# Kernel tuning notes

Hardware: AMD Instinct MI355X
Metric: run time of the kernel (lower is better)

Reference implementation:

```python
import jax, jax.numpy as jnp
import numpy as np

N = 4096
DIN, DOUT, HID, CUTS = 16, 16, 16, 8
RADIUS = 9.0
SCALES = (1.0, 2.0, 3.0, 5.0, 10.0)
REG = 0.01
CHUNK = 512
GROUPS = 4
DINF = DIN + 2 * len(SCALES)  # 26


def leaky(v):
    return jnp.where(v >= 0, v, 0.2 * v)


def sqdist(a, b):
    d2 = jnp.sum(a * a, -1)[:, None] + jnp.sum(b * b, -1)[None, :] - 2.0 * (a @ b.T)
    return jnp.maximum(d2, 0.0)


def tangent_vectors(n):
    # Duff et al. branchless orthonormal basis, as in dMaSIF geometry_processing
    x, y, z = n[..., 0], n[..., 1], n[..., 2]
    s = jnp.where(z >= 0, 1.0, -1.0)
    a = -1.0 / (s + z)
    b = x * y * a
    t1 = jnp.stack([1.0 + s * x * x * a, s * b, -s * x], -1)
    t2 = jnp.stack([b, s + y * y * a, -y], -1)
    return jnp.stack([t1, t2], axis=-2)  # (..., 2, 3)


def group_norm(x, w, b, eps=1e-5):
    # torch GroupNorm(4, C) applied on (1, C, N): normalize over (C/G, N) per group
    n, c = x.shape
    xt = x.T.reshape(GROUPS, c // GROUPS, n)
    m = jnp.mean(xt, axis=(1, 2), keepdims=True)
    v = jnp.mean((xt - m) ** 2, axis=(1, 2), keepdims=True)
    xt = (xt - m) / jnp.sqrt(v + eps)
    return (xt.reshape(c, n) * w[:, None] + b[:, None]).T


def curvature_features(verts, normals):
    # dMaSIF curvatures(): per-scale Gaussian-window covariances, shape operator S = PPt^-1 PQt
    # Pairwise sums factorized into matmuls with the (N,N) window (no (N,N,8) intermediates).
    n_pts = verts.shape[0]
    d2 = sqdist(verts, verts)
    xx = (verts[:, :, None] * verts[:, None, :]).reshape(n_pts, 9)
    feats = []
    for s in SCALES:
        w = jnp.exp(-d2 / (2.0 * s * s))
        u_n = w @ normals  # scale-smoothed normals
        ns = u_n / jnp.maximum(jnp.linalg.norm(u_n, axis=-1, keepdims=True), 1e-12)
        uv = tangent_vectors(ns)  # (N,2,3)
        s0 = jnp.sum(w, 1)
        sx = w @ verts
        sn = w @ ns
        sxx = (w @ xx).reshape(n_pts, 3, 3)
        xn = (verts[:, :, None] * ns[:, None, :]).reshape(n_pts, 9)
        sxn = (w @ xn).reshape(n_pts, 3, 3)
        # sum_j w_ij (x_j-x_i)(x_j-x_i)^T  and  sum_j w_ij (x_j-x_i)(n_j-n_i)^T
        cxx = sxx - verts[:, :, None] * sx[:, None, :] - sx[:, :, None] * verts[:, None, :] \
              + s0[:, None, None] * verts[:, :, None] * verts[:, None, :]
        cxn = sxn - verts[:, :, None] * sn[:, None, :] - sx[:, :, None] * ns[:, None, :] \
              + s0[:, None, None] * verts[:, :, None] * ns[:, None, :]
        ppt = jnp.einsum('nka,nab,nlb->nkl', uv, cxx, uv) + REG * jnp.eye(2, dtype=verts.dtype)
        pqt = jnp.einsum('nka,nab,nlb->nkl', uv, cxn, uv)
        S = jnp.linalg.solve(ppt, pqt)  # (N,2,2)
        feats.append(jnp.clip(S[:, 0, 0] + S[:, 1, 1], -1.0, 1.0))            # mean curvature
        feats.append(jnp.clip(S[:, 0, 0] * S[:, 1, 1] - S[:, 0, 1] * S[:, 1, 0], -1.0, 1.0))  # gauss
    return jnp.stack(feats, -1)  # (N, 2*len(SCALES))


def _forward(verts, vnormals, x, os_w1, os_b1, os_w2, os_b2,
             ni_w1, ni_b1, ni_w2, ni_b2, gn_in_w, gn_in_b,
             cv_a1, cv_b1, cv_a2, cv_b2, no_w1, no_b1, no_w2, no_b2,
             gn_out_w, gn_out_b, ll_w1, ll_b1, ll_w2, ll_b2, lt_w, lt_b):
    curv = curvature_features(verts, vnormals)
    xf = jnp.concatenate([x, curv], axis=-1)  # (N, DINF)
    w = leaky(xf @ os_w1.T + os_b1) @ os_w2.T + os_b2  # orientation scores (N,1)

    # --- load_mesh: steer tangent frames along the gradient of w ---
    p = verts / RADIUS
    ndot = vnormals @ vnormals.T
    W = jnp.exp(-sqdist(p, p) * (2.0 - ndot) ** 2)  # pseudo-geodesic Gaussian window
    uv = tangent_vectors(vnormals)  # (N,2,3)
    ov3 = W @ (w * p) - (W @ w) * p  # sum_j W_ij w_j (x_j - x_i), factorized
    ov = jnp.einsum('nkd,nd->nk', uv, ov3) + 1e-5
    u = ov / jnp.sqrt(jnp.sum(ov * ov, -1, keepdims=True))
    ex, ey = u[:, 0:1], u[:, 1:2]
    u0, v0 = uv[:, 0], uv[:, 1]
    nuv = jnp.concatenate([vnormals[:, None, :],
                           (ex * u0 + ey * v0)[:, None, :],
                           (-ey * u0 + ex * v0)[:, None, :]], axis=1)  # (N,3,3)

    # --- dMaSIFConv layer ---
    h = leaky(leaky(xf @ ni_w1.T + ni_b1) @ ni_w2.T + ni_b2)
    h = group_norm(h, gn_in_w, gn_in_b)  # (N, HID)
    n_all = nuv[:, 0]
    nc = N // CHUNK
    pc = p.reshape(nc, CHUNK, 3)
    nuvc = nuv.reshape(nc, CHUNK, 3, 3)

    def block(args):
        pi, nuvi = args  # (C,3), (C,3,3)
        dx = p[None, :, :] - pi[:, None, :]  # (C,N,3)
        d2 = jnp.sum(dx * dx, -1)
        win = jnp.exp(-d2 * (2.0 - nuvi[:, 0] @ n_all.T) ** 2)  # (C,N)
        X = jnp.einsum('ckd,cnd->cnk', nuvi, dx)  # local coords (C,N,3)
        y = jax.nn.relu(X @ cv_a1.T + cv_b1) @ cv_a2.T + cv_b2  # filter MLP (C,N,HID)
        return jnp.einsum('cn,cnh,nh->ch', win, y, h)

    xi = jax.lax.map(jax.checkpoint(block), (pc, nuvc)).reshape(N, HID)
    xi = group_norm(leaky(leaky(xi @ no_w1.T + no_b1) @ no_w2.T + no_b2), gn_out_w, gn_out_b)
    xi = jax.nn.relu(xi @ ll_w1.T + ll_b1) @ ll_w2.T + ll_b2  # linear_layers[0]
    return xf @ lt_w.T + lt_b + xi  # linear_transform skip + conv branch


def setup_inputs():
    key = jax.random.key(0)
    ks = jax.random.split(key, 20)

    def lin(k, o, i):
        wk = jax.random.fold_in(k, 0)
        bk = jax.random.fold_in(k, 1)
        return ((1.0 / np.sqrt(i)) * jax.random.normal(wk, (o, i)),
                0.01 * jax.random.normal(bk, (o,)))

    verts = 10.0 * jax.random.normal(ks[0], (N, 3))
    vn = jax.random.normal(ks[1], (N, 3))
    vnormals = vn / jnp.linalg.norm(vn, axis=-1, keepdims=True)
    x = jax.random.normal(ks[2], (N, DIN))
    os_w1, os_b1 = lin(ks[3], DOUT, DINF)
    os_w2, os_b2 = lin(ks[4], 1, DOUT)
    ni_w1, ni_b1 = lin(ks[5], HID, DINF)
    ni_w2, ni_b2 = lin(ks[6], HID, HID)
    cv_a1 = jax.random.normal(ks[7], (CUTS, 3))
    cv_b1 = jax.random.uniform(ks[8], (CUTS,)) * 0.8 * jnp.sqrt(jnp.sum(cv_a1 ** 2, -1))
    cv_a2 = jax.random.uniform(ks[9], (HID, CUTS), minval=-1.0, maxval=1.0) / np.sqrt(CUTS)
    cv_b2 = jax.random.normal(ks[10], (HID,)) * 0.5 * jnp.sqrt(jnp.sum(cv_a2 ** 2, -1))
    no_w1, no_b1 = lin(ks[11], DOUT, HID)
    no_w2, no_b2 = lin(ks[12], DOUT, DOUT)
    ll_w1, ll_b1 = lin(ks[13], DOUT, DOUT)
    ll_w2, ll_b2 = lin(ks[14], DOUT, DOUT)
    lt_w, lt_b = lin(ks[15], DOUT, DINF)
    return {'verts': verts, 'vnormals': vnormals, 'x': x,
            'os_w1': os_w1, 'os_b1': os_b1, 'os_w2': os_w2, 'os_b2': os_b2,
            'ni_w1': ni_w1, 'ni_b1': ni_b1, 'ni_w2': ni_w2, 'ni_b2': ni_b2,
            'gn_in_w': jnp.ones(HID), 'gn_in_b': jnp.zeros(HID),
            'cv_a1': cv_a1, 'cv_b1': cv_b1, 'cv_a2': cv_a2, 'cv_b2': cv_b2,
            'no_w1': no_w1, 'no_b1': no_b1, 'no_w2': no_w2, 'no_b2': no_b2,
            'gn_out_w': jnp.ones(DOUT), 'gn_out_b': jnp.zeros(DOUT),
            'll_w1': ll_w1, 'll_b1': ll_b1, 'll_w2': ll_w2, 'll_b2': ll_b2,
            'lt_w': lt_w, 'lt_b': lt_b}


def reference(verts, vnormals, x, os_w1, os_b1, os_w2, os_b2,
              ni_w1, ni_b1, ni_w2, ni_b2, gn_in_w, gn_in_b,
              cv_a1, cv_b1, cv_a2, cv_b2, no_w1, no_b1, no_w2, no_b2,
              gn_out_w, gn_out_b, ll_w1, ll_b1, ll_w2, ll_b2, lt_w, lt_b):
    return _forward(verts, vnormals, x, os_w1, os_b1, os_w2, os_b2,
                    ni_w1, ni_b1, ni_w2, ni_b2, gn_in_w, gn_in_b,
                    cv_a1, cv_b1, cv_a2, cv_b2, no_w1, no_b1, no_w2, no_b2,
                    gn_out_w, gn_out_b, ll_w1, ll_b1, ll_w2, ll_b2, lt_w, lt_b)
```

## Files before the change

### kernel.cpp

```cpp
#include <hip/hip_runtime.h>
#include <hip/hip_bf16.h>
#include <math.h>

#define NPTS 4096
#define DINF 26
#define LOG2E 1.44269504088896f
#define CSTR 72

typedef float f32x4v __attribute__((ext_vector_type(4)));
typedef __bf16 bf16x8v __attribute__((ext_vector_type(8)));

__device__ __forceinline__ float ldb(const float* p, int i){ return p[i]; }
__device__ __forceinline__ float lk(float v){ return v >= 0.0f ? v : 0.2f*v; }
__device__ __forceinline__ float wsum64(float v){
#pragma unroll
  for(int o=32;o>0;o>>=1) v += __shfl_down(v,o);
  return v;
}
__device__ __forceinline__ unsigned short f2bf(float f){
  return __builtin_bit_cast(unsigned short, __float2bfloat16(f));
}
__device__ __forceinline__ float bf2f(unsigned short u){
  return __bfloat162float(__builtin_bit_cast(__hip_bfloat16, u));
}
__device__ __forceinline__ void wave_lds_fence(){
  __builtin_amdgcn_wave_barrier();
  __builtin_amdgcn_s_waitcnt(0xC07F);
  __builtin_amdgcn_wave_barrier();
}
__device__ __forceinline__ void tangent(float nx,float ny,float nz,float* t1,float* t2){
  float s = (nz >= 0.0f) ? 1.0f : -1.0f;
  float a = -1.0f/(s+nz);
  float b = nx*ny*a;
  t1[0]=1.0f+s*nx*nx*a; t1[1]=s*b; t1[2]=-s*nx;
  t2[0]=b; t2[1]=s+ny*ny*a; t2[2]=-ny;
}

__global__ __launch_bounds__(256) void k0_convert(const float* __restrict__ verts,
                                                  const float* __restrict__ vnorm,
                                                  const float* __restrict__ x,
                                                  float* __restrict__ vertsF,
                                                  float* __restrict__ nF,
                                                  float* __restrict__ pF,
                                                  float* __restrict__ xfF){
  int i = blockIdx.x*blockDim.x + threadIdx.x;
  if(i >= NPTS) return;
#pragma unroll
  for(int d=0;d<3;d++){
    float v = verts[i*3+d];
    vertsF[i*3+d]=v;
    pF[i*3+d]=v*(1.0f/9.0f);
    nF[i*3+d]=vnorm[i*3+d];
  }
#pragma unroll
  for(int c=0;c<16;c++) xfF[i*DINF+c]=x[i*16+c];
}

__global__ __launch_bounds__(512) void k1m(const float* __restrict__ vertsF,
                                           const float* __restrict__ nF,
                                           float* __restrict__ sc){
  __shared__ __align__(16) unsigned short fbh[8][16][CSTR];
  __shared__ __align__(16) unsigned short fbl[8][16][CSTR];
  __shared__ __align__(16) float vq[8][64][4];
  __shared__ float red[8][16][16];
  const float c2e[5] = {0.5f*LOG2E, 0.125f*LOG2E, (1.0f/18.0f)*LOG2E,
                        0.02f*LOG2E, 0.005f*LOG2E};
  int lane = threadIdx.x & 63, w = threadIdx.x >> 6;
  int c16 = lane & 15, q = lane >> 4;
  int it = blockIdx.x >> 1, jh = blockIdx.x & 1;
  int i0 = it*16;
  int ia = i0 + c16;
  float vix=vertsF[ia*3+0], viy=vertsF[ia*3+1], viz=vertsF[ia*3+2];
  float nsqi = vix*vix+viy*viy+viz*viz;
  fbh[w][0][lane]=0x3F80u; fbl[w][0][lane]=0u;
#pragma unroll
  for(int c=13;c<16;c++){ fbh[w][c][lane]=0u; fbl[w][c][lane]=0u; }
  f32x4v acc[5];
#pragma unroll
  for(int s=0;s<5;s++) acc[s] = (f32x4v){0.0f,0.0f,0.0f,0.0f};

  int jbeg = jh*2048 + w*256;
#pragma unroll 1
  for(int jb = jbeg; jb < jbeg+256; jb += 64){
    int j = jb + lane;
    float vx=vertsF[j*3+0], vy=vertsF[j*3+1], vz=vertsF[j*3+2];
    float nx=nF[j*3+0], ny=nF[j*3+1], nz=nF[j*3+2];
    float nsq = vx*vx+vy*vy+vz*vz;
    float fv[13];
    fv[1]=vx; fv[2]=vy; fv[3]=vz;
    fv[4]=vx*vx; fv[5]=vx*vy; fv[6]=vx*vz; fv[7]=vy*vy; fv[8]=vy*vz; fv[9]=vz*vz;
    fv[10]=nx; fv[11]=ny; fv[12]=nz;
#pragma unroll
    for(int c=1;c<13;c++){
      unsigned short h=f2bf(fv[c]);
      fbh[w][c][lane]=h;
      fbl[w][c][lane]=f2bf(fv[c]-bf2f(h));
    }
    *(float4*)&vq[w][lane][0] = make_float4(vx,vy,vz,nsq);
    wave_lds_fence();
#pragma unroll
    for(int q2=0;q2<2;q2++){
      int rb = q2*32 + q*8;
      bf16x8v bh = *(const bf16x8v*)&fbh[w][c16][rb];
      bf16x8v bl = *(const bf16x8v*)&fbl[w][c16][rb];
      bf16x8v af[5];
#pragma unroll
      for(int t=0;t<8;t++){
        float4 vv = *(const float4*)&vq[w][rb+t][0];
        float dot = vix*vv.x + viy*vv.y + viz*vv.z;
        float d2 = fmaxf(nsqi + vv.w - 2.0f*dot, 0.0f);
#pragma unroll
        for(int s=0;s<5;s++)
          af[s][t] = __builtin_bit_cast(__bf16, f2bf(exp2f(-d2*c2e[s])));
      }
#pragma unroll
      for(int s=0;s<5;s++){
        acc[s] = __builtin_amdgcn_mfma_f32_16x16x32_bf16(af[s], bh, acc[s], 0,0,0);
        acc[s] = __builtin_amdgcn_mfma_f32_16x16x32_bf16(af[s], bl, acc[s], 0,0,0);
      }
    }
    wave_lds_fence();
  }
#pragma unroll
  for(int s=0;s<5;s++){
#pragma unroll
    for(int r=0;r<4;r++) red[w][q*4+r][c16] = acc[s][r];
    __syncthreads();
    if(w==0){
      float* base = sc + (size_t)s*13*NPTS;
#pragma unroll
      for(int r=0;r<4;r++){
        int m = q*4+r, i = i0+m;
        float D = 0.0f;
#pragma unroll
        for(int ww=0;ww<8;ww++) D += red[ww][m][c16];
        if(c16==0)       atomicAdd(&base[i], D);
        else if(c16<4)   atomicAdd(&base[NPTS + i*3 + (c16-1)], D);
        else if(c16<10)  atomicAdd(&base[4*NPTS + i*6 + (c16-4)], D);
        else if(c16<13)  atomicAdd(&base[10*NPTS + i*3 + (c16-10)], D);
      }
    }
    __syncthreads();
  }
}

__global__ __launch_bounds__(512) void k2m(const float* __restrict__ vertsF,
                                           const float* __restrict__ sc,
                                           float* __restrict__ mom2){
  __shared__ __align__(16) unsigned short fbh[8][16][CSTR];
  __shared__ __align__(16) unsigned short fbl[8][16][CSTR];
  __shared__ __align__(16) float vq[8][64][4];
  __shared__ float red[8][16][16];
  const float c2e[5] = {0.5f*LOG2E, 0.125f*LOG2E, (1.0f/18.0f)*LOG2E,
                        0.02f*LOG2E, 0.005f*LOG2E};
  int lane = threadIdx.x & 63, w = threadIdx.x >> 6;
  int c16 = lane & 15, q = lane >> 4;
  int it = blockIdx.x >> 1, jh = blockIdx.x & 1;
  int i0 = it*16;
  int ia = i0 + c16;
  float vix=vertsF[ia*3+0], viy=vertsF[ia*3+1], viz=vertsF[ia*3+2];
  float nsqi = vix*vix+viy*viy+viz*viz;
#pragma unroll
  for(int c=12;c<16;c++){ fbh[w][c][lane]=0u; fbl[w][c][lane]=0u; }
  f32x4v acc[5];
#pragma unroll
  for(int s=0;s<5;s++) acc[s] = (f32x4v){0.0f,0.0f,0.0f,0.0f};

  int jbeg = jh*2048 + w*256;
#pragma unroll 1
  for(int jb = jbeg; jb < jbeg+256; jb += 64){
    int j = jb + lane;
    float vx=vertsF[j*3+0], vy=vertsF[j*3+1], vz=vertsF[j*3+2];
    float nsq = vx*vx+vy*vy+vz*vz;
    *(float4*)&vq[w][lane][0] = make_float4(vx,vy,vz,nsq);
    wave_lds_fence();
    float d2c[2][8];
#pragma unroll
    for(int q2=0;q2<2;q2++)
#pragma unroll
      for(int t=0;t<8;t++){
        float4 vv = *(const float4*)&vq[w][q2*32+q*8+t][0];
        float dot = vix*vv.x + viy*vv.y + viz*vv.z;
        d2c[q2][t] = fmaxf(nsqi + vv.w - 2.0f*dot, 0.0f);
      }
    wave_lds_fence();
#pragma unroll
    for(int s=0;s<5;s++){
      const float* ub = sc + (size_t)s*13*NPTS + 10*NPTS + (size_t)j*3;
      float ux=ub[0], uy=ub[1], uz=ub[2];
      float inv = 1.0f/fmaxf(sqrtf(ux*ux+uy*uy+uz*uz), 1e-12f);
      float n0=ux*inv, n1=uy*inv, n2=uz*inv;
      float fv[12];
      fv[0]=n0; fv[1]=n1; fv[2]=n2;
      fv[3]=vx*n0; fv[4]=vx*n1; fv[5]=vx*n2;
      fv[6]=vy*n0; fv[7]=vy*n1; fv[8]=vy*n2;
      fv[9]=vz*n0; fv[10]=vz*n1; fv[11]=vz*n2;
#pragma unroll
      for(int c=0;c<12;c++){
        unsigned short h=f2bf(fv[c]);
        fbh[w][c][lane]=h;
        fbl[w][c][lane]=f2bf(fv[c]-bf2f(h));
      }
      wave_lds_fence();
#pragma unroll
      for(int q2=0;q2<2;q2++){
        int rb = q2*32 + q*8;
        bf16x8v bh = *(const bf16x8v*)&fbh[w][c16][rb];
        bf16x8v bl = *(const bf16x8v*)&fbl[w][c16][rb];
        bf16x8v af;
#pragma unroll
        for(int t=0;t<8;t++)
          af[t] = __builtin_bit_cast(__bf16, f2bf(exp2f(-d2c[q2][t]*c2e[s])));
        acc[s] = __builtin_amdgcn_mfma_f32_16x16x32_bf16(af, bh, acc[s], 0,0,0);
        acc[s] = __builtin_amdgcn_mfma_f32_16x16x32_bf16(af, bl, acc[s], 0,0,0);
      }
      wave_lds_fence();
    }
  }
#pragma unroll
  for(int s=0;s<5;s++){
#pragma unroll
    for(int r=0;r<4;r++) red[w][q*4+r][c16] = acc[s][r];
    __syncthreads();
    if(w==0){
#pragma unroll
      for(int r=0;r<4;r++){
        int m = q*4+r, i = i0+m;
        float D = 0.0f;
#pragma unroll
        for(int ww=0;ww<8;ww++) D += red[ww][m][c16];
        if(c16<12) atomicAdd(&mom2[((size_t)s*NPTS + i)*12 + c16], D);
      }
    }
    __syncthreads();
  }
}

__global__ __launch_bounds__(256) void k2s(const float* __restrict__ vertsF,
                                           const float* __restrict__ sc,
                                           const float* __restrict__ mom2,
                                           float* __restrict__ xfF){
  int idx = blockIdx.x*256 + threadIdx.x;
  int i = idx & (NPTS-1);
  int s = idx >> 12;
  const float* base = sc + (size_t)s*13*NPTS;
  float v[3] = { vertsF[i*3+0], vertsF[i*3+1], vertsF[i*3+2] };
  float s0 = base[i];
  float sx[3] = { base[NPTS+i*3+0], base[NPTS+i*3+1], base[NPTS+i*3+2] };
  float sxx6[6];
#pragma unroll
  for(int k=0;k<6;k++) sxx6[k]=base[4*NPTS+i*6+k];
  float ux=base[10*NPTS+i*3+0], uy=base[10*NPTS+i*3+1], uz=base[10*NPTS+i*3+2];
  float invn = 1.0f/fmaxf(sqrtf(ux*ux+uy*uy+uz*uz), 1e-12f);
  float nsi[3] = { ux*invn, uy*invn, uz*invn };
  const float* M2 = mom2 + ((size_t)s*NPTS + i)*12;
  float sn[3] = { M2[0], M2[1], M2[2] };
  float sxn[3][3];
#pragma unroll
  for(int a=0;a<3;a++)
#pragma unroll
    for(int b=0;b<3;b++) sxn[a][b]=M2[3+a*3+b];
  const int m6[3][3]={{0,1,2},{1,3,4},{2,4,5}};
  float cxx[3][3], cxn[3][3];
#pragma unroll
  for(int a=0;a<3;a++)
#pragma unroll
    for(int b=0;b<3;b++){
      cxx[a][b]=sxx6[m6[a][b]] - v[a]*sx[b] - sx[a]*v[b] + s0*v[a]*v[b];
      cxn[a][b]=sxn[a][b]    - v[a]*sn[b] - sx[a]*nsi[b] + s0*v[a]*nsi[b];
    }
  float t1[3],t2[3];
  tangent(nsi[0],nsi[1],nsi[2],t1,t2);
  float ppt[2][2], pqt[2][2];
#pragma unroll
  for(int k=0;k<2;k++){
    const float* tk = (k==0)?t1:t2;
#pragma unroll
    for(int l=0;l<2;l++){
      const float* tl = (l==0)?t1:t2;
      float accx=0.0f, accn=0.0f;
#pragma unroll
      for(int a=0;a<3;a++)
#pragma unroll
        for(int b=0;b<3;b++){
          accx += tk[a]*cxx[a][b]*tl[b];
          accn += tk[a]*cxn[a][b]*tl[b];
        }
      ppt[k][l]=accx + ((k==l)?0.01f:0.0f);
      pqt[k][l]=accn;
    }
  }
  float det = ppt[0][0]*ppt[1][1]-ppt[0][1]*ppt[1][0];
  float id = 1.0f/det;
  float S00=( ppt[1][1]*pqt[0][0]-ppt[0][1]*pqt[1][0])*id;
  float S01=( ppt[1][1]*pqt[0][1]-ppt[0][1]*pqt[1][1])*id;
  float S10=(-ppt[1][0]*pqt[0][0]+ppt[0][0]*pqt[1][0])*id;
  float S11=(-ppt[1][0]*pqt[0][1]+ppt[0][0]*pqt[1][1])*id;
  float f0=fminf(fmaxf(S00+S11,-1.0f),1.0f);
  float f1=fminf(fmaxf(S00*S11-S01*S10,-1.0f),1.0f);
  xfF[i*DINF+16+2*s]=f0;
  xfF[i*DINF+17+2*s]=f1;
}

__global__ __launch_bounds__(256) void k3_mlps(const float* __restrict__ xfF,
    const float* os_w1, const float* os_b1, const float* os_w2, const float* os_b2,
    const float* ni_w1, const float* ni_b1, const float* ni_w2, const float* ni_b2,
    float* __restrict__ wOS, float* __restrict__ hPre, float* __restrict__ stats){
  int i = blockIdx.x*256 + threadIdx.x;
  int lane = threadIdx.x & 63;
  float xf[DINF];
#pragma unroll
  for(int k=0;k<DINF;k++) xf[k]=xfF[i*DINF+k];
  float h1[16];
#pragma unroll
  for(int o=0;o<16;o++){
    float t=ldb(os_b1,o);
#pragma unroll
    for(int k=0;k<DINF;k++) t += xf[k]*ldb(os_w1,o*DINF+k);
    h1[o]=lk(t);
  }
  float w=ldb(os_b2,0);
#pragma unroll
  for(int o=0;o<16;o++) w += h1[o]*ldb(os_w2,o);
  wOS[i]=w;
#pragma unroll
  for(int o=0;o<16;o++){
    float t=ldb(ni_b1,o);
#pragma unroll
    for(int k=0;k<DINF;k++) t += xf[k]*ldb(ni_w1,o*DINF+k);
    h1[o]=lk(t);
  }
  float h2[16];
#pragma unroll
  for(int o=0;o<16;o++){
    float t=ldb(ni_b2,o);
#pragma unroll
    for(int k=0;k<16;k++) t += h1[k]*ldb(ni_w2,o*16+k);
    h2[o]=lk(t);
    hPre[i*16+o]=h2[o];
  }
  float gs[4]={0,0,0,0}, gq[4]={0,0,0,0};
#pragma unroll
  for(int c=0;c<16;c++){ gs[c>>2]+=h2[c]; gq[c>>2]+=h2[c]*h2[c]; }
  __shared__ float ls[8];
  if(threadIdx.x<8) ls[threadIdx.x]=0.0f;
  __syncthreads();
#pragma unroll
  for(int g=0;g<4;g++){ gs[g]=wsum64(gs[g]); gq[g]=wsum64(gq[g]); }
  if(lane==0){
#pragma unroll
    for(int g=0;g<4;g++){ atomicAdd(&ls[2*g],gs[g]); atomicAdd(&ls[2*g+1],gq[g]); }
  }
  __syncthreads();
  if(threadIdx.x<8) atomicAdd(&stats[threadIdx.x], ls[threadIdx.x]);
}

__global__ __launch_bounds__(256) void k3c_gn(const float* __restrict__ hPre,
                                              const float* __restrict__ stats,
                                              const float* gw, const float* gb,
                                              unsigned short* __restrict__ hTb){
  int i = blockIdx.x*256 + threadIdx.x;
  float m[4], r[4];
#pragma unroll
  for(int g=0;g<4;g++){
    float mean = stats[2*g]*(1.0f/(4.0f*NPTS));
    float var  = stats[2*g+1]*(1.0f/(4.0f*NPTS)) - mean*mean;
    m[g]=mean; r[g]=1.0f/sqrtf(var+1e-5f);
  }
#pragma unroll
  for(int c=0;c<16;c++){
    int g=c>>2;
    float v=(hPre[i*16+c]-m[g])*r[g]*ldb(gw,c)+ldb(gb,c);
    hTb[c*NPTS+i]=f2bf(v);
  }
}

__global__ __launch_bounds__(256) void k4_ov(const float* __restrict__ pF,
                                             const float* __restrict__ nF,
                                             const float* __restrict__ wOS,
                                             float* __restrict__ nuvF){
  __shared__ float part[4][4];
  int lane = threadIdx.x & 63;
  int w = threadIdx.x >> 6;
  int ii = w >> 1, jh = w & 1;
  int i = blockIdx.x*2 + ii;
  float pix=pF[i*3+0], piy=pF[i*3+1], piz=pF[i*3+2];
  float nix=nF[i*3+0], niy=nF[i*3+1], niz=nF[i*3+2];
  float a0=0,a1=0,a2=0,a3=0;
#pragma unroll 1
  for(int j=jh*2048+lane; j<jh*2048+2048; j+=64){
    float px=pF[j*3+0], py=pF[j*3+1], pz=pF[j*3+2];
    float nx=nF[j*3+0], ny=nF[j*3+1], nz=nF[j*3+2];
    float wj=wOS[j];
    float dx=px-pix, dy=py-piy, dz=pz-piz;
    float d2=dx*dx+dy*dy+dz*dz;
    float f=2.0f-(nx*nix+ny*niy+nz*niz);
    float Wv=__expf(-d2*f*f);
    float Ww=Wv*wj;
    a0+=Ww*px; a1+=Ww*py; a2+=Ww*pz; a3+=Ww;
  }
  a0=wsum64(a0); a1=wsum64(a1); a2=wsum64(a2); a3=wsum64(a3);
  if(lane==0){ part[w][0]=a0; part[w][1]=a1; part[w][2]=a2; part[w][3]=a3; }
  __syncthreads();
  if(lane==0 && jh==0){
    a0=part[w][0]+part[w+1][0]; a1=part[w][1]+part[w+1][1];
    a2=part[w][2]+part[w+1][2]; a3=part[w][3]+part[w+1][3];
    float o0=a0-a3*pix, o1=a1-a3*piy, o2=a2-a3*piz;
    float t1[3],t2[3];
    tangent(nix,niy,niz,t1,t2);
    float ov0=t1[0]*o0+t1[1]*o1+t1[2]*o2+1e-5f;
    float ov1=t2[0]*o0+t2[1]*o1+t2[2]*o2+1e-5f;
    float inv=1.0f/sqrtf(ov0*ov0+ov1*ov1);
    float ex=ov0*inv, ey=ov1*inv;
    nuvF[i*9+0]=nix; nuvF[i*9+1]=niy; nuvF[i*9+2]=niz;
    nuvF[i*9+3]= ex*t1[0]+ey*t2[0]; nuvF[i*9+4]= ex*t1[1]+ey*t2[1]; nuvF[i*9+5]= ex*t1[2]+ey*t2[2];
    nuvF[i*9+6]=-ey*t1[0]+ex*t2[0]; nuvF[i*9+7]=-ey*t1[1]+ex*t2[1]; nuvF[i*9+8]=-ey*t1[2]+ex*t2[2];
  }
}

__global__ __launch_bounds__(256) void k5_conv(const float* __restrict__ pF,
                                               const float* __restrict__ nF,
                                               const float* __restrict__ nuvF,
                                               const unsigned short* __restrict__ hTb,
                                               const float* cv_a1, const float* cv_b1,
                                               const float* cv_a2, const float* cv_b2,
                                               float* __restrict__ xiF){
  __shared__ __align__(16) unsigned short zs[4][16][CSTR];
  __shared__ float red[4][64][4];
  int lane = threadIdx.x & 63;
  int w = threadIdx.x >> 6;
  int ii = w >> 1, jh = w & 1;
  int i = blockIdx.x*2 + ii;
  int c16 = lane & 15, q = lane >> 4;
#pragma unroll
  for(int c=9;c<16;c++) zs[w][c][lane]=0u;

  float pix=pF[i*3+0], piy=pF[i*3+1], piz=pF[i*3+2];
  float nu[9];
#pragma unroll
  for(int k=0;k<9;k++) nu[k]=nuvF[i*9+k];
  float a1w[8][3], b1w[8];
#pragma unroll
  for(int c=0;c<8;c++){
    a1w[c][0]=cv_a1[c*3+0]; a1w[c][1]=cv_a1[c*3+1]; a1w[c][2]=cv_a1[c*3+2];
    b1w[c]=cv_b1[c];
  }
  const unsigned short* hrow = hTb + c16*NPTS;
  f32x4v acc = {0.0f,0.0f,0.0f,0.0f};
  wave_lds_fence();

#pragma unroll 1
  for(int jb=jh*2048; jb<jh*2048+2048; jb+=64){
    int j = jb + lane;
    float px=pF[j*3+0], py=pF[j*3+1], pz=pF[j*3+2];
    float nx=nF[j*3+0], ny=nF[j*3+1], nz=nF[j*3+2];
    float dx=px-pix, dy=py-piy, dz=pz-piz;
    float d2=dx*dx+dy*dy+dz*dz;
    float f=2.0f-(nx*nu[0]+ny*nu[1]+nz*nu[2]);
    float win=__expf(-d2*f*f);
    float X0=nu[0]*dx+nu[1]*dy+nu[2]*dz;
    float X1=nu[3]*dx+nu[4]*dy+nu[5]*dz;
    float X2=nu[6]*dx+nu[7]*dy+nu[8]*dz;
#pragma unroll
    for(int c=0;c<8;c++){
      float r=fmaf(X0,a1w[c][0],fmaf(X1,a1w[c][1],fmaf(X2,a1w[c][2],b1w[c])));
      zs[w][c][lane]=f2bf(win*fmaxf(r,0.0f));
    }
    zs[w][8][lane]=f2bf(win);
    wave_lds_fence();
#pragma unroll
    for(int q2=0;q2<2;q2++){
      int jb2 = jb + q2*32;
      bf16x8v afr = *(const bf16x8v*)(hrow + jb2 + q*8);
      bf16x8v bfr = *(const bf16x8v*)&zs[w][c16][q2*32 + q*8];
      acc = __builtin_amdgcn_mfma_f32_16x16x32_bf16(afr, bfr, acc, 0, 0, 0);
    }
    wave_lds_fence();
  }
#pragma unroll
  for(int r=0;r<4;r++) red[w][lane][r]=acc[r];
  __syncthreads();
  if(jh==0){
#pragma unroll
    for(int r=0;r<4;r++){
      int h = q*4 + r;
      float coef = (c16<8) ? cv_a2[h*8+c16] : ((c16==8) ? cv_b2[h] : 0.0f);
      float v = (red[w][lane][r]+red[w+1][lane][r])*coef;
#pragma unroll
      for(int o=1;o<16;o<<=1) v += __shfl_xor(v,o);
      if(c16==0) xiF[i*16+h]=v;
    }
  }
}

__global__ __launch_bounds__(256) void k6a(const float* __restrict__ xiF,
    const float* no_w1, const float* no_b1, const float* no_w2, const float* no_b2,
    float* __restrict__ tF, float* __restrict__ stats2){
  int i = blockIdx.x*256 + threadIdx.x;
  int lane = threadIdx.x & 63;
  float xi[16];
#pragma unroll
  for(int k=0;k<16;k++) xi[k]=xiF[i*16+k];
  float t1[16];
#pragma unroll
  for(int o=0;o<16;o++){
    float t=ldb(no_b1,o);
#pragma unroll
    for(int k=0;k<16;k++) t += xi[k]*ldb(no_w1,o*16+k);
    t1[o]=lk(t);
  }
  float t2[16];
#pragma unroll
  for(int o=0;o<16;o++){
    float t=ldb(no_b2,o);
#pragma unroll
    for(int k=0;k<16;k++) t += t1[k]*ldb(no_w2,o*16+k);
    t2[o]=lk(t);
    tF[i*16+o]=t2[o];
  }
  float gs[4]={0,0,0,0}, gq[4]={0,0,0,0};
#pragma unroll
  for(int c=0;c<16;c++){ gs[c>>2]+=t2[c]; gq[c>>2]+=t2[c]*t2[c]; }
  __shared__ float ls[8];
  if(threadIdx.x<8) ls[threadIdx.x]=0.0f;
  __syncthreads();
#pragma unroll
  for(int g=0;g<4;g++){ gs[g]=wsum64(gs[g]); gq[g]=wsum64(gq[g]); }
  if(lane==0){
#pragma unroll
    for(int g=0;g<4;g++){ atomicAdd(&ls[2*g],gs[g]); atomicAdd(&ls[2*g+1],gq[g]); }
  }
  __syncthreads();
  if(threadIdx.x<8) atomicAdd(&stats2[threadIdx.x], ls[threadIdx.x]);
}

__global__ __launch_bounds__(256) void k6c(const float* __restrict__ tF,
    const float* __restrict__ xfF, const float* __restrict__ stats2,
    const float* gw, const float* gb,
    const float* ll_w1, const float* ll_b1, const float* ll_w2, const float* ll_b2,
    const float* lt_w, const float* lt_b,
    float* __restrict__ out){
  int i = blockIdx.x*256 + threadIdx.x;
  float m[4], r[4];
#pragma unroll
  for(int g=0;g<4;g++){
    float mean = stats2[2*g]*(1.0f/(4.0f*NPTS));
    float var  = stats2[2*g+1]*(1.0f/(4.0f*NPTS)) - mean*mean;
    m[g]=mean; r[g]=1.0f/sqrtf(var+1e-5f);
  }
  float tn[16];
#pragma unroll
  for(int c=0;c<16;c++){
    int g=c>>2;
    tn[c]=(tF[i*16+c]-m[g])*r[g]*ldb(gw,c)+ldb(gb,c);
  }
  float z1[16];
#pragma unroll
  for(int o=0;o<16;o++){
    float t=ldb(ll_b1,o);
#pragma unroll
    for(int k=0;k<16;k++) t += tn[k]*ldb(ll_w1,o*16+k);
    z1[o]=fmaxf(t,0.0f);
  }
  float xf[DINF];
#pragma unroll
  for(int k=0;k<DINF;k++) xf[k]=xfF[i*DINF+k];
#pragma unroll
  for(int o=0;o<16;o++){
    float z=ldb(ll_b2,o);
#pragma unroll
    for(int k=0;k<16;k++) z += z1[k]*ldb(ll_w2,o*16+k);
    float lt=ldb(lt_b,o);
#pragma unroll
    for(int k=0;k<DINF;k++) lt += xf[k]*ldb(lt_w,o*DINF+k);
    out[i*16+o]=z+lt;
  }
}

extern "C" void kernel_launch(void* const* d_in, const int* in_sizes, int n_in,
                              void* d_out, int out_size, void* d_ws, size_t ws_size,
                              hipStream_t stream){
  const float* verts    = (const float*)d_in[0];
  const float* vnormals = (const float*)d_in[1];
  const float* x        = (const float*)d_in[2];
  const float* os_w1    = (const float*)d_in[3];
  const float* os_b1    = (const float*)d_in[4];
  const float* os_w2    = (const float*)d_in[5];
  const float* os_b2    = (const float*)d_in[6];
  const float* ni_w1    = (const float*)d_in[7];
  const float* ni_b1    = (const float*)d_in[8];
  const float* ni_w2    = (const float*)d_in[9];
  const float* ni_b2    = (const float*)d_in[10];
  const float* gn_in_w  = (const float*)d_in[11];
  const float* gn_in_b  = (const float*)d_in[12];
  const float* cv_a1    = (const float*)d_in[13];
  const float* cv_b1    = (const float*)d_in[14];
  const float* cv_a2    = (const float*)d_in[15];
  const float* cv_b2    = (const float*)d_in[16];
  const float* no_w1    = (const float*)d_in[17];
  const float* no_b1    = (const float*)d_in[18];
  const float* no_w2    = (const float*)d_in[19];
  const float* no_b2    = (const float*)d_in[20];
  const float* gn_out_w = (const float*)d_in[21];
  const float* gn_out_b = (const float*)d_in[22];
  const float* ll_w1    = (const float*)d_in[23];
  const float* ll_b1    = (const float*)d_in[24];
  const float* ll_w2    = (const float*)d_in[25];
  const float* ll_b2    = (const float*)d_in[26];
  const float* lt_w     = (const float*)d_in[27];
  const float* lt_b     = (const float*)d_in[28];

  float* W = (float*)d_ws;
  size_t off = 0;
  float* vertsF = W + off; off += (size_t)3*NPTS;
  float* nF     = W + off; off += (size_t)3*NPTS;
  float* pF     = W + off; off += (size_t)3*NPTS;
  float* xfF    = W + off; off += (size_t)DINF*NPTS;
  float* sc     = W + off; off += (size_t)13*NPTS*5;
  float* wOS    = W + off; off += (size_t)NPTS;
  float* hPre   = W + off; off += (size_t)16*NPTS;
  unsigned short* hTb = (unsigned short*)(W + off); off += (size_t)8*NPTS;
  float* nuvF   = W + off; off += (size_t)9*NPTS;
  float* xiF    = W + off; off += (size_t)16*NPTS;
  float* tF     = W + off; off += (size_t)16*NPTS;
  float* stats  = W + off; off += 16;
  float* mom2 = hPre;

  hipMemsetAsync(stats, 0, 16*sizeof(float), stream);
  hipMemsetAsync(sc,   0, (size_t)13*NPTS*5*sizeof(float), stream);
  hipMemsetAsync(mom2, 0, (size_t)12*NPTS*5*sizeof(float), stream);

  k0_convert<<<NPTS/256, 256, 0, stream>>>(verts, vnormals, x, vertsF, nF, pF, xfF);
  k1m<<<NPTS/8, 512, 0, stream>>>(vertsF, nF, sc);
  k2m<<<NPTS/8, 512, 0, stream>>>(vertsF, sc, mom2);
  k2s<<<5*NPTS/256, 256, 0, stream>>>(vertsF, sc, mom2, xfF);
  k3_mlps<<<NPTS/256, 256, 0, stream>>>(xfF, os_w1, os_b1, os_w2, os_b2,
                                        ni_w1, ni_b1, ni_w2, ni_b2, wOS, hPre, stats);
  k3c_gn<<<NPTS/256, 256, 0, stream>>>(hPre, stats, gn_in_w, gn_in_b, hTb);
  k4_ov<<<NPTS/2, 256, 0, stream>>>(pF, nF, wOS, nuvF);
  k5_conv<<<NPTS/2, 256, 0, stream>>>(pF, nF, nuvF, hTb, cv_a1, cv_b1, cv_a2, cv_b2, xiF);
  k6a<<<NPTS/256, 256, 0, stream>>>(xiF, no_w1, no_b1, no_w2, no_b2, tF, stats+8);
  k6c<<<NPTS/256, 256, 0, stream>>>(tF, xfF, stats+8, gn_out_w, gn_out_b,
                                    ll_w1, ll_b1, ll_w2, ll_b2, lt_w, lt_b, (float*)d_out);
}
```

Baseline: 342.2 us.

## Retile conv kernel to 16 points per block with split-j partial sums

The quasi-geodesic conv kernel now processes 16 target points per block instead of one per wave pair. Each lane owns one target point and builds per-channel window-weighted features straight into MFMA A fragments, using 9 accumulators, while neighbour positions and normals are staged through LDS. The j range is split across 4 blocks per tile. Each block writes its partial result to a separate buffer, and k6a sums the partials, which removes the per-point feature LDS round trip and spreads the work over more blocks. In exchange it uses more accumulator registers, does redundant per-lane exp work laid out differently, and needs extra workspace and memory traffic for the partials.

New measurement: 309.7 us. 9.5% less time.

```diff
diff --git a/kernel.cpp b/kernel.cpp
--- a/kernel.cpp
+++ b/kernel.cpp
@@ -6,6 +6,7 @@
 #define DINF 26
 #define LOG2E 1.44269504088896f
 #define CSTR 72
+#define JSPL 4
 
 typedef float f32x4v __attribute__((ext_vector_type(4)));
 typedef __bf16 bf16x8v __attribute__((ext_vector_type(8)));
@@ -424,17 +425,14 @@
                                                const unsigned short* __restrict__ hTb,
                                                const float* cv_a1, const float* cv_b1,
                                                const float* cv_a2, const float* cv_b2,
-                                               float* __restrict__ xiF){
-  __shared__ __align__(16) unsigned short zs[4][16][CSTR];
+                                               float* __restrict__ xiP){
+  __shared__ __align__(16) float vq[4][64][8];
   __shared__ float red[4][64][4];
-  int lane = threadIdx.x & 63;
-  int w = threadIdx.x >> 6;
-  int ii = w >> 1, jh = w & 1;
-  int i = blockIdx.x*2 + ii;
+  int lane = threadIdx.x & 63, w = threadIdx.x >> 6;
   int c16 = lane & 15, q = lane >> 4;
-#pragma unroll
-  for(int c=9;c<16;c++) zs[w][c][lane]=0u;
-
+  int it = blockIdx.x >> 2, jseg = blockIdx.x & (JSPL-1);
+  int i0 = it*16;
+  int i = i0 + c16;
   float pix=pF[i*3+0], piy=pF[i*3+1], piz=pF[i*3+2];
   float nu[9];
 #pragma unroll
@@ -445,62 +443,82 @@
     a1w[c][0]=cv_a1[c*3+0]; a1w[c][1]=cv_a1[c*3+1]; a1w[c][2]=cv_a1[c*3+2];
     b1w[c]=cv_b1[c];
   }
-  const unsigned short* hrow = hTb + c16*NPTS;
-  f32x4v acc = {0.0f,0.0f,0.0f,0.0f};
-  wave_lds_fence();
-
+  f32x4v acc[9];
+#pragma unroll
+  for(int c=0;c<9;c++) acc[c]=(f32x4v){0.0f,0.0f,0.0f,0.0f};
+
+  int jbeg = jseg*(NPTS/JSPL) + w*(NPTS/JSPL/4);
+  int jend = jbeg + (NPTS/JSPL/4);
 #pragma unroll 1
-  for(int jb=jh*2048; jb<jh*2048+2048; jb+=64){
+  for(int jb=jbeg; jb<jend; jb+=64){
     int j = jb + lane;
-    float px=pF[j*3+0], py=pF[j*3+1], pz=pF[j*3+2];
-    float nx=nF[j*3+0], ny=nF[j*3+1], nz=nF[j*3+2];
-    float dx=px-pix, dy=py-piy, dz=pz-piz;
-    float d2=dx*dx+dy*dy+dz*dz;
-    float f=2.0f-(nx*nu[0]+ny*nu[1]+nz*nu[2]);
-    float win=__expf(-d2*f*f);
-    float X0=nu[0]*dx+nu[1]*dy+nu[2]*dz;
-    float X1=nu[3]*dx+nu[4]*dy+nu[5]*dz;
-    float X2=nu[6]*dx+nu[7]*dy+nu[8]*dz;
-#pragma unroll
-    for(int c=0;c<8;c++){
-      float r=fmaf(X0,a1w[c][0],fmaf(X1,a1w[c][1],fmaf(X2,a1w[c][2],b1w[c])));
-      zs[w][c][lane]=f2bf(win*fmaxf(r,0.0f));
-    }
-    zs[w][8][lane]=f2bf(win);
+    *(float4*)&vq[w][lane][0] = make_float4(pF[j*3+0],pF[j*3+1],pF[j*3+2],0.0f);
+    *(float4*)&vq[w][lane][4] = make_float4(nF[j*3+0],nF[j*3+1],nF[j*3+2],0.0f);
     wave_lds_fence();
 #pragma unroll
     for(int q2=0;q2<2;q2++){
       int jb2 = jb + q2*32;
-      bf16x8v afr = *(const bf16x8v*)(hrow + jb2 + q*8);
-      bf16x8v bfr = *(const bf16x8v*)&zs[w][c16][q2*32 + q*8];
-      acc = __builtin_amdgcn_mfma_f32_16x16x32_bf16(afr, bfr, acc, 0, 0, 0);
+      bf16x8v bfr = *(const bf16x8v*)(hTb + c16*NPTS + jb2 + q*8);
+      bf16x8v af[9];
+#pragma unroll
+      for(int t=0;t<8;t++){
+        int rloc = q2*32 + q*8 + t;
+        float4 P  = *(const float4*)&vq[w][rloc][0];
+        float4 Nj = *(const float4*)&vq[w][rloc][4];
+        float dx=P.x-pix, dy=P.y-piy, dz=P.z-piz;
+        float d2=dx*dx+dy*dy+dz*dz;
+        float f=2.0f-(Nj.x*nu[0]+Nj.y*nu[1]+Nj.z*nu[2]);
+        float win=exp2f(-d2*f*f*LOG2E);
+        float X0=nu[0]*dx+nu[1]*dy+nu[2]*dz;
+        float X1=nu[3]*dx+nu[4]*dy+nu[5]*dz;
+        float X2=nu[6]*dx+nu[7]*dy+nu[8]*dz;
+#pragma unroll
+        for(int c=0;c<8;c++){
+          float r=fmaf(X0,a1w[c][0],fmaf(X1,a1w[c][1],fmaf(X2,a1w[c][2],b1w[c])));
+          af[c][t]=__builtin_bit_cast(__bf16, f2bf(win*fmaxf(r,0.0f)));
+        }
+        af[8][t]=__builtin_bit_cast(__bf16, f2bf(win));
+      }
+#pragma unroll
+      for(int c=0;c<9;c++)
+        acc[c] = __builtin_amdgcn_mfma_f32_16x16x32_bf16(af[c], bfr, acc[c], 0,0,0);
     }
     wave_lds_fence();
   }
-#pragma unroll
-  for(int r=0;r<4;r++) red[w][lane][r]=acc[r];
+  float a2row[8];
+#pragma unroll
+  for(int c=0;c<8;c++) a2row[c]=cv_a2[c16*8+c];
+  float b2v = cv_b2[c16];
+#pragma unroll
+  for(int r=0;r<4;r++){
+    float xi = acc[8][r]*b2v;
+#pragma unroll
+    for(int c=0;c<8;c++) xi += acc[c][r]*a2row[c];
+    red[w][lane][r]=xi;
+  }
   __syncthreads();
-  if(jh==0){
+  if(w==0){
 #pragma unroll
     for(int r=0;r<4;r++){
-      int h = q*4 + r;
-      float coef = (c16<8) ? cv_a2[h*8+c16] : ((c16==8) ? cv_b2[h] : 0.0f);
-      float v = (red[w][lane][r]+red[w+1][lane][r])*coef;
-#pragma unroll
-      for(int o=1;o<16;o<<=1) v += __shfl_xor(v,o);
-      if(c16==0) xiF[i*16+h]=v;
-    }
-  }
-}
-
-__global__ __launch_bounds__(256) void k6a(const float* __restrict__ xiF,
+      float v = red[0][lane][r]+red[1][lane][r]+red[2][lane][r]+red[3][lane][r];
+      xiP[((size_t)jseg*NPTS + (i0 + q*4 + r))*16 + c16] = v;
+    }
+  }
+}
+
+__global__ __launch_bounds__(256) void k6a(const float* __restrict__ xiP,
     const float* no_w1, const float* no_b1, const float* no_w2, const float* no_b2,
     float* __restrict__ tF, float* __restrict__ stats2){
   int i = blockIdx.x*256 + threadIdx.x;
   int lane = threadIdx.x & 63;
   float xi[16];
 #pragma unroll
-  for(int k=0;k<16;k++) xi[k]=xiF[i*16+k];
+  for(int k=0;k<16;k++){
+    float v=0.0f;
+#pragma unroll
+    for(int s=0;s<JSPL;s++) v += xiP[((size_t)s*NPTS + i)*16 + k];
+    xi[k]=v;
+  }
   float t1[16];
 #pragma unroll
   for(int o=0;o<16;o++){
@@ -621,7 +639,7 @@
   float* hPre   = W + off; off += (size_t)16*NPTS;
   unsigned short* hTb = (unsigned short*)(W + off); off += (size_t)8*NPTS;
   float* nuvF   = W + off; off += (size_t)9*NPTS;
-  float* xiF    = W + off; off += (size_t)16*NPTS;
+  float* xiP    = W + off; off += (size_t)JSPL*16*NPTS;
   float* tF     = W + off; off += (size_t)16*NPTS;
   float* stats  = W + off; off += 16;
   float* mom2 = hPre;
@@ -638,8 +656,9 @@
                                         ni_w1, ni_b1, ni_w2, ni_b2, wOS, hPre, stats);
   k3c_gn<<<NPTS/256, 256, 0, stream>>>(hPre, stats, gn_in_w, gn_in_b, hTb);
   k4_ov<<<NPTS/2, 256, 0, stream>>>(pF, nF, wOS, nuvF);
-  k5_conv<<<NPTS/2, 256, 0, stream>>>(pF, nF, nuvF, hTb, cv_a1, cv_b1, cv_a2, cv_b2, xiF);
-  k6a<<<NPTS/256, 256, 0, stream>>>(xiF, no_w1, no_b1, no_w2, no_b2, tF, stats+8);
+  k5_conv<<<(NPTS/16)*JSPL, 256, 0, stream>>>(pF, nF, nuvF, hTb,
+                                              cv_a1, cv_b1, cv_a2, cv_b2, xiP);
+  k6a<<<NPTS/256, 256, 0, stream>>>(xiP, no_w1, no_b1, no_w2, no_b2, tF, stats+8);
   k6c<<<NPTS/256, 256, 0, stream>>>(tF, xfF, stats+8, gn_out_w, gn_out_b,
                                     ll_w1, ll_b1, ll_w2, ll_b2, lt_w, lt_b, (float*)d_out);
 }
```
